# Performance work log

Hardware: AMD Instinct MI355X
Metric: run time of the kernel (lower is better)

## Reference

```python
import jax, jax.numpy as jnp
import numpy as np

N_NODES = 50000
N_EDGES = 800000
D_IN = 96
D_OUT = 96


def setup_inputs() -> dict:
    key = jax.random.key(0)
    k1, k2, k3, k4 = jax.random.split(key, 4)
    feat = jax.random.normal(k1, (N_NODES, D_IN), dtype=jnp.float32)
    # xavier_normal-like init for weight, zeros bias (as in the torch module)
    std = (2.0 / (D_IN + D_OUT)) ** 0.5
    weight = jax.random.normal(k2, (D_IN, D_OUT), dtype=jnp.float32) * std
    bias = jnp.zeros((D_OUT,), dtype=jnp.float32)
    src = jax.random.randint(k3, (N_EDGES,), 0, N_NODES, dtype=jnp.int64)
    dst = jax.random.randint(k4, (N_EDGES,), 0, N_NODES, dtype=jnp.int64)
    return {"feat": feat, "weight": weight, "bias": bias, "src": src, "dst": dst}


def reference(feat, weight, bias, src, dst):
    N = feat.shape[0]
    ones = jnp.ones(src.shape[0], dtype=feat.dtype)
    out_deg = jax.ops.segment_sum(ones, src, num_segments=N)  # out-degree per node
    in_deg = jax.ops.segment_sum(ones, dst, num_segments=N)   # in-degree per node
    ci = jnp.clip(out_deg, 1.0, None) ** -0.5                 # src-side norm
    cj = jnp.clip(in_deg, 1.0, None) ** -0.5                  # dst-side norm
    # gather src features * ci, scatter-sum to dst, scale by cj
    msg = feat[src] * ci[src, None]                           # [E, D_IN]
    agg = jax.ops.segment_sum(msg, dst, num_segments=N) * cj[:, None]
    # DGL UDF reduce only updates nodes that receive messages; isolated
    # (zero in-degree) nodes keep their original features.
    h = jnp.where(in_deg[:, None] > 0, agg, feat)
    return jnp.matmul(h, weight) + bias
```

## Files before the change

### kernel.cpp

```cpp
#include <hip/hip_runtime.h>

#define N_NODES 50000
#define N_EDGES 800000
#define D 96
#define D4 (D / 4)

#define HB 128
#define CHUNK (N_EDGES / HB)
#define NW (N_NODES / 4)

#define RL 12
#define NTILES (N_NODES / 16)
#define CONV_BLOCKS ((N_NODES * RL + 255) / 256)
#define WPREP_BLOCKS ((D * (D / 2) + 255) / 256)
#define CSR_CAP (N_EDGES + 8 * N_NODES)

typedef __attribute__((ext_vector_type(8))) short short8;
typedef __attribute__((ext_vector_type(4))) float floatx4;

__device__ __forceinline__ short8 as_short8(uint4 u) { return *(short8*)&u; }

__global__ void __launch_bounds__(1024) hist_kernel(
        const int* __restrict__ src, const int* __restrict__ dst,
        unsigned* __restrict__ hist, unsigned* __restrict__ total) {
    __shared__ unsigned hbin[NW];
    int b = blockIdx.x, t = threadIdx.x;
    if (b == 0 && t == 0) *total = 0;
    int e0 = b * CHUNK;
#pragma unroll 1
    for (int p = 0; p < 2; ++p) {
        const int* __restrict__ arr = (p == 0) ? src : dst;
        for (int i = t; i < NW; i += 1024) hbin[i] = 0;
        __syncthreads();
        for (int i = t; i < CHUNK; i += 1024) {
            int l = arr[e0 + i];
            atomicAdd(&hbin[l >> 2], 1u << ((l & 3) * 8));
        }
        __syncthreads();
        unsigned* __restrict__ g = hist + ((size_t)p * HB + b) * NW;
        for (int i = t; i < NW; i += 1024) g[i] = hbin[i];
        __syncthreads();
    }
}

__global__ void __launch_bounds__(256) reduce_kernel(
        unsigned* __restrict__ hist, float* __restrict__ ci,
        int* __restrict__ deg_in, int* __restrict__ off,
        unsigned* __restrict__ total) {
    int w = blockIdx.x * 256 + threadIdx.x;
    bool valid = w < NW;
    unsigned acc_s = 0;
    int4 dv = {0, 0, 0, 0};
    if (valid) {
        const unsigned* __restrict__ ps = hist + w;
        unsigned* __restrict__ pd = hist + (size_t)HB * NW + w;
#pragma unroll 8
        for (int b = 0; b < HB; ++b) acc_s += ps[(size_t)b * NW];
        unsigned run = 0;
#pragma unroll 4
        for (int b = 0; b < HB; ++b) {
            unsigned v = pd[(size_t)b * NW];
            pd[(size_t)b * NW] = run;
            run += v;
        }
        dv.x = (int)( run        & 0xFFu);
        dv.y = (int)((run >>  8) & 0xFFu);
        dv.z = (int)((run >> 16) & 0xFFu);
        dv.w = (int)( run >> 24        );
    }
    int4 pv;
    pv.x = (dv.x + 7) & ~7;
    pv.y = (dv.y + 7) & ~7;
    pv.z = (dv.z + 7) & ~7;
    pv.w = (dv.w + 7) & ~7;
    int sum4 = pv.x + pv.y + pv.z + pv.w;
    int lane = threadIdx.x & 63;
    int incl = sum4;
#pragma unroll
    for (int st = 1; st < 64; st <<= 1) {
        int v = __shfl_up(incl, st, 64);
        if (lane >= st) incl += v;
    }
    int excl = incl - sum4;
    int wave_total = __shfl(incl, 63, 64);
    int base = 0;
    if (lane == 63) base = (int)atomicAdd(total, (unsigned)wave_total);
    base = __shfl(base, 63, 64);
    if (valid) {
        int n0 = 4 * w;
        int b0 = base + excl;
        int4 ov;
        ov.x = b0;
        ov.y = b0 + pv.x;
        ov.z = b0 + pv.x + pv.y;
        ov.w = b0 + pv.x + pv.y + pv.z;
        *(int4*)&off[n0] = ov;
        *(int4*)&deg_in[n0] = dv;
        float4 cv;
        cv.x = rsqrtf(fmaxf((float)( acc_s        & 0xFFu), 1.0f));
        cv.y = rsqrtf(fmaxf((float)((acc_s >>  8) & 0xFFu), 1.0f));
        cv.z = rsqrtf(fmaxf((float)((acc_s >> 16) & 0xFFu), 1.0f));
        cv.w = rsqrtf(fmaxf((float)( acc_s >> 24        ), 1.0f));
        *(float4*)&ci[n0] = cv;
    }
}

__device__ __forceinline__ unsigned bf16pack(float a, float b) {
    unsigned ua = __float_as_uint(a);
    unsigned ub = __float_as_uint(b);
    ua = (ua + 0x7FFFu + ((ua >> 16) & 1u)) >> 16;
    ub = (ub + 0x7FFFu + ((ub >> 16) & 1u)) & 0xFFFF0000u;
    return ua | ub;
}

__global__ void __launch_bounds__(256) conv_kernel(
        const float4* __restrict__ feat4, const float* __restrict__ ci,
        uint4* __restrict__ sfeat, const float* __restrict__ W,
        unsigned* __restrict__ WT32) {
    int blk = blockIdx.x;
    if (blk >= CONV_BLOCKS) {
        int t = (blk - CONV_BLOCKS) * 256 + threadIdx.x;
        if (t >= D * (D / 2)) return;
        int n = t / (D / 2);
        int j = t - n * (D / 2);
        float w0 = W[(2 * j) * D + n];
        float w1 = W[(2 * j + 1) * D + n];
        WT32[n * (D / 2) + j] = bf16pack(w0, w1);
        return;
    }
    int t = blk * 256 + threadIdx.x;
    if (t >= N_NODES * RL) return;
    int n = t / RL;
    int lane = t - n * RL;
    float c = ci[n];
    float4 a = feat4[n * D4 + lane * 2];
    float4 b = feat4[n * D4 + lane * 2 + 1];
    uint4 o;
    o.x = bf16pack(a.x * c, a.y * c);
    o.y = bf16pack(a.z * c, a.w * c);
    o.z = bf16pack(b.x * c, b.y * c);
    o.w = bf16pack(b.z * c, b.w * c);
    sfeat[t] = o;
}

__global__ void __launch_bounds__(1024) fill_kernel(
        const int* __restrict__ src, const int* __restrict__ dst,
        const int* __restrict__ off, const unsigned* __restrict__ hist,
        unsigned short* __restrict__ csr) {
    __shared__ unsigned cur[NW];
    int b = blockIdx.x, t = threadIdx.x;
    const unsigned* __restrict__ pr = hist + ((size_t)HB + b) * NW;
    for (int i = t; i < NW; i += 1024) cur[i] = pr[i];
    __syncthreads();
    int e0 = b * CHUNK;
    for (int i = t; i < CHUNK; i += 1024) {
        int d = dst[e0 + i];
        int sh = (d & 3) * 8;
        unsigned old = atomicAdd(&cur[d >> 2], 1u << sh);
        int pos = (int)((old >> sh) & 0xFFu);
        csr[off[d] + pos] = (unsigned short)src[e0 + i];
    }
}

__global__ void __launch_bounds__(192) gather_kernel(
        const float4* __restrict__ feat4, const uint4* __restrict__ sfeat,
        const int* __restrict__ deg_in, const int* __restrict__ off,
        const unsigned short* __restrict__ csr, uint4* __restrict__ hbuf) {
    int tid = threadIdx.x;
    int g = tid / RL;
    int lane = tid - g * RL;
    int n = blockIdx.x * 16 + g;
    int deg = deg_in[n];
    uint4* __restrict__ hout = hbuf + (size_t)n * RL + lane;
    if (deg == 0) {
        float4 a = feat4[n * D4 + lane * 2];
        float4 b = feat4[n * D4 + lane * 2 + 1];
        uint4 o;
        o.x = bf16pack(a.x, a.y);
        o.y = bf16pack(a.z, a.w);
        o.z = bf16pack(b.x, b.y);
        o.w = bf16pack(b.z, b.w);
        *hout = o;
        return;
    }
    const unsigned short* __restrict__ bk = csr + off[n];
    const uint4* __restrict__ sf = sfeat + lane;
    float acc[8] = {};
#define ACC8(v)  { \
    acc[0] += __uint_as_float((v).x << 16); \
    acc[1] += __uint_as_float((v).x & 0xFFFF0000u); \
    acc[2] += __uint_as_float((v).y << 16); \
    acc[3] += __uint_as_float((v).y & 0xFFFF0000u); \
    acc[4] += __uint_as_float((v).z << 16); \
    acc[5] += __uint_as_float((v).z & 0xFFFF0000u); \
    acc[6] += __uint_as_float((v).w << 16); \
    acc[7] += __uint_as_float((v).w & 0xFFFF0000u); }
    int full = deg & ~7;
    int i = 0;
    for (; i < full; i += 8) {
        uint4 idx = *(const uint4*)(bk + i);
        unsigned s0 = idx.x & 0xFFFFu, s1 = idx.x >> 16;
        unsigned s2 = idx.y & 0xFFFFu, s3 = idx.y >> 16;
        unsigned s4 = idx.z & 0xFFFFu, s5 = idx.z >> 16;
        unsigned s6 = idx.w & 0xFFFFu, s7 = idx.w >> 16;
        uint4 v0 = sf[(size_t)s0 * RL];
        uint4 v1 = sf[(size_t)s1 * RL];
        uint4 v2 = sf[(size_t)s2 * RL];
        uint4 v3 = sf[(size_t)s3 * RL];
        uint4 v4 = sf[(size_t)s4 * RL];
        uint4 v5 = sf[(size_t)s5 * RL];
        uint4 v6 = sf[(size_t)s6 * RL];
        uint4 v7 = sf[(size_t)s7 * RL];
        ACC8(v0); ACC8(v1); ACC8(v2); ACC8(v3);
        ACC8(v4); ACC8(v5); ACC8(v6); ACC8(v7);
    }
    for (; i < deg; ++i) {
        uint4 v = sf[(size_t)bk[i] * RL];
        ACC8(v);
    }
#undef ACC8
    float cj = rsqrtf((float)deg);
    uint4 o;
    o.x = bf16pack(acc[0] * cj, acc[1] * cj);
    o.y = bf16pack(acc[2] * cj, acc[3] * cj);
    o.z = bf16pack(acc[4] * cj, acc[5] * cj);
    o.w = bf16pack(acc[6] * cj, acc[7] * cj);
    *hout = o;
}

__global__ void __launch_bounds__(256) mfma_mm_kernel(
        const uint4* __restrict__ hb4, const uint4* __restrict__ wt4,
        const float* __restrict__ bias, float* __restrict__ out) {
    int wave = threadIdx.x >> 6;
    int lane = threadIdx.x & 63;
    int tile = blockIdx.x * 4 + wave;
    if (tile >= NTILES) return;
    int m = lane & 15, quad = lane >> 4;
    int row0 = tile * 16;
    int rb = (row0 + m) * RL + quad;
    short8 a0 = as_short8(hb4[rb]);
    short8 a1 = as_short8(hb4[rb + 4]);
    short8 a2 = as_short8(hb4[rb + 8]);
    int r_out0 = row0 + quad * 4;
#pragma unroll
    for (int ct = 0; ct < 6; ++ct) {
        int n = ct * 16 + m;
        int wb = n * RL + quad;
        short8 b0 = as_short8(wt4[wb]);
        short8 b1 = as_short8(wt4[wb + 4]);
        short8 b2 = as_short8(wt4[wb + 8]);
        floatx4 c = {0.f, 0.f, 0.f, 0.f};
        c = __builtin_amdgcn_mfma_f32_16x16x32_bf16(a0, b0, c, 0, 0, 0);
        c = __builtin_amdgcn_mfma_f32_16x16x32_bf16(a1, b1, c, 0, 0, 0);
        c = __builtin_amdgcn_mfma_f32_16x16x32_bf16(a2, b2, c, 0, 0, 0);
        float bs = bias[n];
#pragma unroll
        for (int r = 0; r < 4; ++r)
            out[(size_t)(r_out0 + r) * D + n] = c[r] + bs;
    }
}

extern "C" void kernel_launch(void* const* d_in, const int* in_sizes, int n_in,
                              void* d_out, int out_size, void* d_ws, size_t ws_size,
                              hipStream_t stream) {
    const float* feat = (const float*)d_in[0];
    const float* W    = (const float*)d_in[1];
    const float* bias = (const float*)d_in[2];
    const int*   src  = (const int*)d_in[3];
    const int*   dst  = (const int*)d_in[4];

    unsigned*       hist   = (unsigned*)d_ws;
    float*          ci     = (float*)(hist + (size_t)2 * HB * NW);
    int*            off    = (int*)(ci + N_NODES);
    int*            deg_in = off + N_NODES;
    unsigned short* csr    = (unsigned short*)(deg_in + N_NODES);
    uint4*          sfeat  = (uint4*)((char*)csr + ((size_t)CSR_CAP * 2 + 15 & ~15));
    uint4*          hbuf   = sfeat + (size_t)N_NODES * RL;
    unsigned*       WT32   = (unsigned*)(hbuf + (size_t)N_NODES * RL);
    unsigned*       total  = WT32 + D * (D / 2);

    hist_kernel<<<HB, 1024, 0, stream>>>(src, dst, hist, total);
    reduce_kernel<<<(NW + 255) / 256, 256, 0, stream>>>(hist, ci, deg_in, off, total);
    conv_kernel<<<CONV_BLOCKS + WPREP_BLOCKS, 256, 0, stream>>>(
        (const float4*)feat, ci, sfeat, W, WT32);
    fill_kernel<<<HB, 1024, 0, stream>>>(src, dst, off, hist, csr);
    gather_kernel<<<N_NODES / 16, 192, 0, stream>>>(
        (const float4*)feat, sfeat, deg_in, off, csr, hbuf);
    mfma_mm_kernel<<<(NTILES + 3) / 4, 256, 0, stream>>>(
        hbuf, (const uint4*)WT32, bias, (float*)d_out);
}
```

Before: 159.7 us.

## Fuse reduce with feature conversion and gather with MFMA matmul

Merges the degree-reduce/offset kernel with the bf16 feature scaling pass, keeping ci in shared memory so the ci buffer round-trip and one launch go away. Also fuses the gather-aggregate with the MFMA matmul: each 192-thread block writes its 16 aggregated rows into padded LDS, and its 3 waves each compute 2 of the 6 output column tiles, so the hbuf buffer and another launch disappear. The trade-off is a reduce/convert kernel with only ~49 blocks, each converting 1024 nodes serially, which can cut parallelism for the streaming conversion. The gather blocks also now carry extra matmul work.

```diff
diff --git a/kernel.cpp b/kernel.cpp
--- a/kernel.cpp
+++ b/kernel.cpp
@@ -10,15 +10,22 @@
 #define NW (N_NODES / 4)
 
 #define RL 12
-#define NTILES (N_NODES / 16)
-#define CONV_BLOCKS ((N_NODES * RL + 255) / 256)
-#define WPREP_BLOCKS ((D * (D / 2) + 255) / 256)
+#define HPAD 13
+#define RC_BLOCKS ((NW + 255) / 256)
 #define CSR_CAP (N_EDGES + 8 * N_NODES)
 
 typedef __attribute__((ext_vector_type(8))) short short8;
 typedef __attribute__((ext_vector_type(4))) float floatx4;
 
 __device__ __forceinline__ short8 as_short8(uint4 u) { return *(short8*)&u; }
+
+__device__ __forceinline__ unsigned bf16pack(float a, float b) {
+    unsigned ua = __float_as_uint(a);
+    unsigned ub = __float_as_uint(b);
+    ua = (ua + 0x7FFFu + ((ua >> 16) & 1u)) >> 16;
+    ub = (ub + 0x7FFFu + ((ub >> 16) & 1u)) & 0xFFFF0000u;
+    return ua | ub;
+}
 
 __global__ void __launch_bounds__(1024) hist_kernel(
         const int* __restrict__ src, const int* __restrict__ dst,
@@ -43,11 +50,24 @@
     }
 }
 
-__global__ void __launch_bounds__(256) reduce_kernel(
-        unsigned* __restrict__ hist, float* __restrict__ ci,
-        int* __restrict__ deg_in, int* __restrict__ off,
-        unsigned* __restrict__ total) {
-    int w = blockIdx.x * 256 + threadIdx.x;
+__global__ void __launch_bounds__(256) reduce_conv_kernel(
+        unsigned* __restrict__ hist, const float4* __restrict__ feat4,
+        const float* __restrict__ W, int* __restrict__ deg_in,
+        int* __restrict__ off, unsigned* __restrict__ total,
+        uint4* __restrict__ sfeat, unsigned* __restrict__ WT32) {
+    int b = blockIdx.x, tid = threadIdx.x;
+    if (b == RC_BLOCKS) {
+        for (int t = tid; t < D * (D / 2); t += 256) {
+            int n = t / (D / 2);
+            int j = t - n * (D / 2);
+            float w0 = W[(2 * j) * D + n];
+            float w1 = W[(2 * j + 1) * D + n];
+            WT32[n * (D / 2) + j] = bf16pack(w0, w1);
+        }
+        return;
+    }
+    __shared__ float ci_s[1024];
+    int w = b * 256 + tid;
     bool valid = w < NW;
     unsigned acc_s = 0;
     int4 dv = {0, 0, 0, 0};
@@ -55,12 +75,12 @@
         const unsigned* __restrict__ ps = hist + w;
         unsigned* __restrict__ pd = hist + (size_t)HB * NW + w;
 #pragma unroll 8
-        for (int b = 0; b < HB; ++b) acc_s += ps[(size_t)b * NW];
+        for (int bb = 0; bb < HB; ++bb) acc_s += ps[(size_t)bb * NW];
         unsigned run = 0;
 #pragma unroll 4
-        for (int b = 0; b < HB; ++b) {
-            unsigned v = pd[(size_t)b * NW];
-            pd[(size_t)b * NW] = run;
+        for (int bb = 0; bb < HB; ++bb) {
+            unsigned v = pd[(size_t)bb * NW];
+            pd[(size_t)bb * NW] = run;
             run += v;
         }
         dv.x = (int)( run        & 0xFFu);
@@ -74,7 +94,7 @@
     pv.z = (dv.z + 7) & ~7;
     pv.w = (dv.w + 7) & ~7;
     int sum4 = pv.x + pv.y + pv.z + pv.w;
-    int lane = threadIdx.x & 63;
+    int lane = tid & 63;
     int incl = sum4;
 #pragma unroll
     for (int st = 1; st < 64; st <<= 1) {
@@ -101,46 +121,25 @@
         cv.y = rsqrtf(fmaxf((float)((acc_s >>  8) & 0xFFu), 1.0f));
         cv.z = rsqrtf(fmaxf((float)((acc_s >> 16) & 0xFFu), 1.0f));
         cv.w = rsqrtf(fmaxf((float)( acc_s >> 24        ), 1.0f));
-        *(float4*)&ci[n0] = cv;
-    }
-}
-
-__device__ __forceinline__ unsigned bf16pack(float a, float b) {
-    unsigned ua = __float_as_uint(a);
-    unsigned ub = __float_as_uint(b);
-    ua = (ua + 0x7FFFu + ((ua >> 16) & 1u)) >> 16;
-    ub = (ub + 0x7FFFu + ((ub >> 16) & 1u)) & 0xFFFF0000u;
-    return ua | ub;
-}
-
-__global__ void __launch_bounds__(256) conv_kernel(
-        const float4* __restrict__ feat4, const float* __restrict__ ci,
-        uint4* __restrict__ sfeat, const float* __restrict__ W,
-        unsigned* __restrict__ WT32) {
-    int blk = blockIdx.x;
-    if (blk >= CONV_BLOCKS) {
-        int t = (blk - CONV_BLOCKS) * 256 + threadIdx.x;
-        if (t >= D * (D / 2)) return;
-        int n = t / (D / 2);
-        int j = t - n * (D / 2);
-        float w0 = W[(2 * j) * D + n];
-        float w1 = W[(2 * j + 1) * D + n];
-        WT32[n * (D / 2) + j] = bf16pack(w0, w1);
-        return;
-    }
-    int t = blk * 256 + threadIdx.x;
-    if (t >= N_NODES * RL) return;
-    int n = t / RL;
-    int lane = t - n * RL;
-    float c = ci[n];
-    float4 a = feat4[n * D4 + lane * 2];
-    float4 b = feat4[n * D4 + lane * 2 + 1];
-    uint4 o;
-    o.x = bf16pack(a.x * c, a.y * c);
-    o.y = bf16pack(a.z * c, a.w * c);
-    o.z = bf16pack(b.x * c, b.y * c);
-    o.w = bf16pack(b.z * c, b.w * c);
-    sfeat[t] = o;
+        *(float4*)&ci_s[4 * tid] = cv;
+    }
+    __syncthreads();
+    int nbase = b * 1024;
+    int cnt = min(1024, N_NODES - nbase);
+    for (int i = tid; i < cnt * RL; i += 256) {
+        int nl = i / RL;
+        int lane2 = i - nl * RL;
+        int n = nbase + nl;
+        float c = ci_s[nl];
+        float4 a = feat4[n * D4 + lane2 * 2];
+        float4 bb = feat4[n * D4 + lane2 * 2 + 1];
+        uint4 o;
+        o.x = bf16pack(a.x * c, a.y * c);
+        o.y = bf16pack(a.z * c, a.w * c);
+        o.z = bf16pack(bb.x * c, bb.y * c);
+        o.w = bf16pack(bb.z * c, bb.w * c);
+        sfeat[(size_t)n * RL + lane2] = o;
+    }
 }
 
 __global__ void __launch_bounds__(1024) fill_kernel(
@@ -162,88 +161,85 @@
     }
 }
 
-__global__ void __launch_bounds__(192) gather_kernel(
+__global__ void __launch_bounds__(192) gather_mm_kernel(
         const float4* __restrict__ feat4, const uint4* __restrict__ sfeat,
         const int* __restrict__ deg_in, const int* __restrict__ off,
-        const unsigned short* __restrict__ csr, uint4* __restrict__ hbuf) {
+        const unsigned short* __restrict__ csr, const uint4* __restrict__ wt4,
+        const float* __restrict__ bias, float* __restrict__ out) {
+    __shared__ uint4 sh[16 * HPAD];
     int tid = threadIdx.x;
-    int g = tid / RL;
-    int lane = tid - g * RL;
-    int n = blockIdx.x * 16 + g;
-    int deg = deg_in[n];
-    uint4* __restrict__ hout = hbuf + (size_t)n * RL + lane;
-    if (deg == 0) {
-        float4 a = feat4[n * D4 + lane * 2];
-        float4 b = feat4[n * D4 + lane * 2 + 1];
-        uint4 o;
-        o.x = bf16pack(a.x, a.y);
-        o.y = bf16pack(a.z, a.w);
-        o.z = bf16pack(b.x, b.y);
-        o.w = bf16pack(b.z, b.w);
-        *hout = o;
-        return;
-    }
-    const unsigned short* __restrict__ bk = csr + off[n];
-    const uint4* __restrict__ sf = sfeat + lane;
-    float acc[8] = {};
+    {
+        int g = tid / RL;
+        int lane = tid - g * RL;
+        int n = blockIdx.x * 16 + g;
+        int deg = deg_in[n];
+        uint4* __restrict__ hout = &sh[g * HPAD + lane];
+        if (deg == 0) {
+            float4 a = feat4[n * D4 + lane * 2];
+            float4 b = feat4[n * D4 + lane * 2 + 1];
+            uint4 o;
+            o.x = bf16pack(a.x, a.y);
+            o.y = bf16pack(a.z, a.w);
+            o.z = bf16pack(b.x, b.y);
+            o.w = bf16pack(b.z, b.w);
+            *hout = o;
+        } else {
+            const unsigned short* __restrict__ bk = csr + off[n];
+            const uint4* __restrict__ sf = sfeat + lane;
+            float acc[8] = {};
 #define ACC8(v)  { \
-    acc[0] += __uint_as_float((v).x << 16); \
-    acc[1] += __uint_as_float((v).x & 0xFFFF0000u); \
-    acc[2] += __uint_as_float((v).y << 16); \
-    acc[3] += __uint_as_float((v).y & 0xFFFF0000u); \
-    acc[4] += __uint_as_float((v).z << 16); \
-    acc[5] += __uint_as_float((v).z & 0xFFFF0000u); \
-    acc[6] += __uint_as_float((v).w << 16); \
-    acc[7] += __uint_as_float((v).w & 0xFFFF0000u); }
-    int full = deg & ~7;
-    int i = 0;
-    for (; i < full; i += 8) {
-        uint4 idx = *(const uint4*)(bk + i);
-        unsigned s0 = idx.x & 0xFFFFu, s1 = idx.x >> 16;
-        unsigned s2 = idx.y & 0xFFFFu, s3 = idx.y >> 16;
-        unsigned s4 = idx.z & 0xFFFFu, s5 = idx.z >> 16;
-        unsigned s6 = idx.w & 0xFFFFu, s7 = idx.w >> 16;
-        uint4 v0 = sf[(size_t)s0 * RL];
-        uint4 v1 = sf[(size_t)s1 * RL];
-        uint4 v2 = sf[(size_t)s2 * RL];
-        uint4 v3 = sf[(size_t)s3 * RL];
-        uint4 v4 = sf[(size_t)s4 * RL];
-        uint4 v5 = sf[(size_t)s5 * RL];
-        uint4 v6 = sf[(size_t)s6 * RL];
-        uint4 v7 = sf[(size_t)s7 * RL];
-        ACC8(v0); ACC8(v1); ACC8(v2); ACC8(v3);
-        ACC8(v4); ACC8(v5); ACC8(v6); ACC8(v7);
-    }
-    for (; i < deg; ++i) {
-        uint4 v = sf[(size_t)bk[i] * RL];
-        ACC8(v);
-    }
+        acc[0] += __uint_as_float((v).x << 16); \
+        acc[1] += __uint_as_float((v).x & 0xFFFF0000u); \
+        acc[2] += __uint_as_float((v).y << 16); \
+        acc[3] += __uint_as_float((v).y & 0xFFFF0000u); \
+        acc[4] += __uint_as_float((v).z << 16); \
+        acc[5] += __uint_as_float((v).z & 0xFFFF0000u); \
+        acc[6] += __uint_as_float((v).w << 16); \
+        acc[7] += __uint_as_float((v).w & 0xFFFF0000u); }
+            int full = deg & ~7;
+            int i = 0;
+            for (; i < full; i += 8) {
+                uint4 idx = *(const uint4*)(bk + i);
+                unsigned s0 = idx.x & 0xFFFFu, s1 = idx.x >> 16;
+                unsigned s2 = idx.y & 0xFFFFu, s3 = idx.y >> 16;
+                unsigned s4 = idx.z & 0xFFFFu, s5 = idx.z >> 16;
+                unsigned s6 = idx.w & 0xFFFFu, s7 = idx.w >> 16;
+                uint4 v0 = sf[(size_t)s0 * RL];
+                uint4 v1 = sf[(size_t)s1 * RL];
+                uint4 v2 = sf[(size_t)s2 * RL];
+                uint4 v3 = sf[(size_t)s3 * RL];
+                uint4 v4 = sf[(size_t)s4 * RL];
+                uint4 v5 = sf[(size_t)s5 * RL];
+                uint4 v6 = sf[(size_t)s6 * RL];
+                uint4 v7 = sf[(size_t)s7 * RL];
+                ACC8(v0); ACC8(v1); ACC8(v2); ACC8(v3);
+                ACC8(v4); ACC8(v5); ACC8(v6); ACC8(v7);
+            }
+            for (; i < deg; ++i) {
+                uint4 v = sf[(size_t)bk[i] * RL];
+                ACC8(v);
+            }
 #undef ACC8
-    float cj = rsqrtf((float)deg);
-    uint4 o;
-    o.x = bf16pack(acc[0] * cj, acc[1] * cj);
-    o.y = bf16pack(acc[2] * cj, acc[3] * cj);
-    o.z = bf16pack(acc[4] * cj, acc[5] * cj);
-    o.w = bf16pack(acc[6] * cj, acc[7] * cj);
-    *hout = o;
-}
-
-__global__ void __launch_bounds__(256) mfma_mm_kernel(
-        const uint4* __restrict__ hb4, const uint4* __restrict__ wt4,
-        const float* __restrict__ bias, float* __restrict__ out) {
-    int wave = threadIdx.x >> 6;
-    int lane = threadIdx.x & 63;
-    int tile = blockIdx.x * 4 + wave;
-    if (tile >= NTILES) return;
+            float cj = rsqrtf((float)deg);
+            uint4 o;
+            o.x = bf16pack(acc[0] * cj, acc[1] * cj);
+            o.y = bf16pack(acc[2] * cj, acc[3] * cj);
+            o.z = bf16pack(acc[4] * cj, acc[5] * cj);
+            o.w = bf16pack(acc[6] * cj, acc[7] * cj);
+            *hout = o;
+        }
+    }
+    __syncthreads();
+    int wave = tid >> 6;
+    int lane = tid & 63;
     int m = lane & 15, quad = lane >> 4;
-    int row0 = tile * 16;
-    int rb = (row0 + m) * RL + quad;
-    short8 a0 = as_short8(hb4[rb]);
-    short8 a1 = as_short8(hb4[rb + 4]);
-    short8 a2 = as_short8(hb4[rb + 8]);
+    short8 a0 = as_short8(sh[m * HPAD + quad]);
+    short8 a1 = as_short8(sh[m * HPAD + 4 + quad]);
+    short8 a2 = as_short8(sh[m * HPAD + 8 + quad]);
+    int row0 = blockIdx.x * 16;
     int r_out0 = row0 + quad * 4;
 #pragma unroll
-    for (int ct = 0; ct < 6; ++ct) {
+    for (int ct = wave * 2; ct < wave * 2 + 2; ++ct) {
         int n = ct * 16 + m;
         int wb = n * RL + quad;
         short8 b0 = as_short8(wt4[wb]);
@@ -270,22 +266,18 @@
     const int*   dst  = (const int*)d_in[4];
 
     unsigned*       hist   = (unsigned*)d_ws;
-    float*          ci     = (float*)(hist + (size_t)2 * HB * NW);
-    int*            off    = (int*)(ci + N_NODES);
+    int*            off    = (int*)(hist + (size_t)2 * HB * NW);
     int*            deg_in = off + N_NODES;
     unsigned short* csr    = (unsigned short*)(deg_in + N_NODES);
-    uint4*          sfeat  = (uint4*)((char*)csr + ((size_t)CSR_CAP * 2 + 15 & ~15));
-    uint4*          hbuf   = sfeat + (size_t)N_NODES * RL;
-    unsigned*       WT32   = (unsigned*)(hbuf + (size_t)N_NODES * RL);
+    uint4*          sfeat  = (uint4*)((char*)csr + (((size_t)CSR_CAP * 2 + 15) & ~(size_t)15));
+    unsigned*       WT32   = (unsigned*)(sfeat + (size_t)N_NODES * RL);
     unsigned*       total  = WT32 + D * (D / 2);
 
     hist_kernel<<<HB, 1024, 0, stream>>>(src, dst, hist, total);
-    reduce_kernel<<<(NW + 255) / 256, 256, 0, stream>>>(hist, ci, deg_in, off, total);
-    conv_kernel<<<CONV_BLOCKS + WPREP_BLOCKS, 256, 0, stream>>>(
-        (const float4*)feat, ci, sfeat, W, WT32);
+    reduce_conv_kernel<<<RC_BLOCKS + 1, 256, 0, stream>>>(
+        hist, (const float4*)feat, W, deg_in, off, total, sfeat, WT32);
     fill_kernel<<<HB, 1024, 0, stream>>>(src, dst, off, hist, csr);
-    gather_kernel<<<N_NODES / 16, 192, 0, stream>>>(
-        (const float4*)feat, sfeat, deg_in, off, csr, hbuf);
-    mfma_mm_kernel<<<(NTILES + 3) / 4, 256, 0, stream>>>(
-        hbuf, (const uint4*)WT32, bias, (float*)d_out);
-}
+    gather_mm_kernel<<<N_NODES / 16, 192, 0, stream>>>(
+        (const float4*)feat, sfeat, deg_in, off, csr, (const uint4*)WT32,
+        bias, (float*)d_out);
+}
```

New measurement: 167.8 us. 5.1% more time.

## Fuse neighbor gather with MFMA projection through shared memory tile

Applied to the files above, without the earlier changes.

The gather kernel now writes its 16-node bf16 aggregate tile into padded shared memory instead of a global buffer. After a barrier, its three waves each compute two 16-column MFMA output tiles, which removes the separate matmul kernel launch and the global round trip of the hidden features. The reduce kernel also moves from 256 to 64 threads per block, so each block is a single wave. The cost is that the matmul work now sits behind the gather's tail latency inside each block, with three waves instead of four per tile.

```diff
diff --git a/kernel.cpp b/kernel.cpp
--- a/kernel.cpp
+++ b/kernel.cpp
@@ -10,7 +10,7 @@
 #define NW (N_NODES / 4)
 
 #define RL 12
-#define NTILES (N_NODES / 16)
+#define HPAD 13
 #define CONV_BLOCKS ((N_NODES * RL + 255) / 256)
 #define WPREP_BLOCKS ((D * (D / 2) + 255) / 256)
 #define CSR_CAP (N_EDGES + 8 * N_NODES)
@@ -19,6 +19,14 @@
 typedef __attribute__((ext_vector_type(4))) float floatx4;
 
 __device__ __forceinline__ short8 as_short8(uint4 u) { return *(short8*)&u; }
+
+__device__ __forceinline__ unsigned bf16pack(float a, float b) {
+    unsigned ua = __float_as_uint(a);
+    unsigned ub = __float_as_uint(b);
+    ua = (ua + 0x7FFFu + ((ua >> 16) & 1u)) >> 16;
+    ub = (ub + 0x7FFFu + ((ub >> 16) & 1u)) & 0xFFFF0000u;
+    return ua | ub;
+}
 
 __global__ void __launch_bounds__(1024) hist_kernel(
         const int* __restrict__ src, const int* __restrict__ dst,
@@ -43,11 +51,11 @@
     }
 }
 
-__global__ void __launch_bounds__(256) reduce_kernel(
+__global__ void __launch_bounds__(64) reduce_kernel(
         unsigned* __restrict__ hist, float* __restrict__ ci,
         int* __restrict__ deg_in, int* __restrict__ off,
         unsigned* __restrict__ total) {
-    int w = blockIdx.x * 256 + threadIdx.x;
+    int w = blockIdx.x * 64 + threadIdx.x;
     bool valid = w < NW;
     unsigned acc_s = 0;
     int4 dv = {0, 0, 0, 0};
@@ -74,7 +82,7 @@
     pv.z = (dv.z + 7) & ~7;
     pv.w = (dv.w + 7) & ~7;
     int sum4 = pv.x + pv.y + pv.z + pv.w;
-    int lane = threadIdx.x & 63;
+    int lane = threadIdx.x;
     int incl = sum4;
 #pragma unroll
     for (int st = 1; st < 64; st <<= 1) {
@@ -105,14 +113,6 @@
     }
 }
 
-__device__ __forceinline__ unsigned bf16pack(float a, float b) {
-    unsigned ua = __float_as_uint(a);
-    unsigned ub = __float_as_uint(b);
-    ua = (ua + 0x7FFFu + ((ua >> 16) & 1u)) >> 16;
-    ub = (ub + 0x7FFFu + ((ub >> 16) & 1u)) & 0xFFFF0000u;
-    return ua | ub;
-}
-
 __global__ void __launch_bounds__(256) conv_kernel(
         const float4* __restrict__ feat4, const float* __restrict__ ci,
         uint4* __restrict__ sfeat, const float* __restrict__ W,
@@ -162,88 +162,85 @@
     }
 }
 
-__global__ void __launch_bounds__(192) gather_kernel(
+__global__ void __launch_bounds__(192) gather_mm_kernel(
         const float4* __restrict__ feat4, const uint4* __restrict__ sfeat,
         const int* __restrict__ deg_in, const int* __restrict__ off,
-        const unsigned short* __restrict__ csr, uint4* __restrict__ hbuf) {
+        const unsigned short* __restrict__ csr, const uint4* __restrict__ wt4,
+        const float* __restrict__ bias, float* __restrict__ out) {
+    __shared__ uint4 sh[16 * HPAD];
     int tid = threadIdx.x;
-    int g = tid / RL;
-    int lane = tid - g * RL;
-    int n = blockIdx.x * 16 + g;
-    int deg = deg_in[n];
-    uint4* __restrict__ hout = hbuf + (size_t)n * RL + lane;
-    if (deg == 0) {
-        float4 a = feat4[n * D4 + lane * 2];
-        float4 b = feat4[n * D4 + lane * 2 + 1];
-        uint4 o;
-        o.x = bf16pack(a.x, a.y);
-        o.y = bf16pack(a.z, a.w);
-        o.z = bf16pack(b.x, b.y);
-        o.w = bf16pack(b.z, b.w);
-        *hout = o;
-        return;
-    }
-    const unsigned short* __restrict__ bk = csr + off[n];
-    const uint4* __restrict__ sf = sfeat + lane;
-    float acc[8] = {};
+    {
+        int g = tid / RL;
+        int lane = tid - g * RL;
+        int n = blockIdx.x * 16 + g;
+        int deg = deg_in[n];
+        uint4* __restrict__ hout = &sh[g * HPAD + lane];
+        if (deg == 0) {
+            float4 a = feat4[n * D4 + lane * 2];
+            float4 b = feat4[n * D4 + lane * 2 + 1];
+            uint4 o;
+            o.x = bf16pack(a.x, a.y);
+            o.y = bf16pack(a.z, a.w);
+            o.z = bf16pack(b.x, b.y);
+            o.w = bf16pack(b.z, b.w);
+            *hout = o;
+        } else {
+            const unsigned short* __restrict__ bk = csr + off[n];
+            const uint4* __restrict__ sf = sfeat + lane;
+            float acc[8] = {};
 #define ACC8(v)  { \
-    acc[0] += __uint_as_float((v).x << 16); \
-    acc[1] += __uint_as_float((v).x & 0xFFFF0000u); \
-    acc[2] += __uint_as_float((v).y << 16); \
-    acc[3] += __uint_as_float((v).y & 0xFFFF0000u); \
-    acc[4] += __uint_as_float((v).z << 16); \
-    acc[5] += __uint_as_float((v).z & 0xFFFF0000u); \
-    acc[6] += __uint_as_float((v).w << 16); \
-    acc[7] += __uint_as_float((v).w & 0xFFFF0000u); }
-    int full = deg & ~7;
-    int i = 0;
-    for (; i < full; i += 8) {
-        uint4 idx = *(const uint4*)(bk + i);
-        unsigned s0 = idx.x & 0xFFFFu, s1 = idx.x >> 16;
-        unsigned s2 = idx.y & 0xFFFFu, s3 = idx.y >> 16;
-        unsigned s4 = idx.z & 0xFFFFu, s5 = idx.z >> 16;
-        unsigned s6 = idx.w & 0xFFFFu, s7 = idx.w >> 16;
-        uint4 v0 = sf[(size_t)s0 * RL];
-        uint4 v1 = sf[(size_t)s1 * RL];
-        uint4 v2 = sf[(size_t)s2 * RL];
-        uint4 v3 = sf[(size_t)s3 * RL];
-        uint4 v4 = sf[(size_t)s4 * RL];
-        uint4 v5 = sf[(size_t)s5 * RL];
-        uint4 v6 = sf[(size_t)s6 * RL];
-        uint4 v7 = sf[(size_t)s7 * RL];
-        ACC8(v0); ACC8(v1); ACC8(v2); ACC8(v3);
-        ACC8(v4); ACC8(v5); ACC8(v6); ACC8(v7);
-    }
-    for (; i < deg; ++i) {
-        uint4 v = sf[(size_t)bk[i] * RL];
-        ACC8(v);
-    }
+        acc[0] += __uint_as_float((v).x << 16); \
+        acc[1] += __uint_as_float((v).x & 0xFFFF0000u); \
+        acc[2] += __uint_as_float((v).y << 16); \
+        acc[3] += __uint_as_float((v).y & 0xFFFF0000u); \
+        acc[4] += __uint_as_float((v).z << 16); \
+        acc[5] += __uint_as_float((v).z & 0xFFFF0000u); \
+        acc[6] += __uint_as_float((v).w << 16); \
+        acc[7] += __uint_as_float((v).w & 0xFFFF0000u); }
+            int full = deg & ~7;
+            int i = 0;
+            for (; i < full; i += 8) {
+                uint4 idx = *(const uint4*)(bk + i);
+                unsigned s0 = idx.x & 0xFFFFu, s1 = idx.x >> 16;
+                unsigned s2 = idx.y & 0xFFFFu, s3 = idx.y >> 16;
+                unsigned s4 = idx.z & 0xFFFFu, s5 = idx.z >> 16;
+                unsigned s6 = idx.w & 0xFFFFu, s7 = idx.w >> 16;
+                uint4 v0 = sf[(size_t)s0 * RL];
+                uint4 v1 = sf[(size_t)s1 * RL];
+                uint4 v2 = sf[(size_t)s2 * RL];
+                uint4 v3 = sf[(size_t)s3 * RL];
+                uint4 v4 = sf[(size_t)s4 * RL];
+                uint4 v5 = sf[(size_t)s5 * RL];
+                uint4 v6 = sf[(size_t)s6 * RL];
+                uint4 v7 = sf[(size_t)s7 * RL];
+                ACC8(v0); ACC8(v1); ACC8(v2); ACC8(v3);
+                ACC8(v4); ACC8(v5); ACC8(v6); ACC8(v7);
+            }
+            for (; i < deg; ++i) {
+                uint4 v = sf[(size_t)bk[i] * RL];
+                ACC8(v);
+            }
 #undef ACC8
-    float cj = rsqrtf((float)deg);
-    uint4 o;
-    o.x = bf16pack(acc[0] * cj, acc[1] * cj);
-    o.y = bf16pack(acc[2] * cj, acc[3] * cj);
-    o.z = bf16pack(acc[4] * cj, acc[5] * cj);
-    o.w = bf16pack(acc[6] * cj, acc[7] * cj);
-    *hout = o;
-}
-
-__global__ void __launch_bounds__(256) mfma_mm_kernel(
-        const uint4* __restrict__ hb4, const uint4* __restrict__ wt4,
-        const float* __restrict__ bias, float* __restrict__ out) {
-    int wave = threadIdx.x >> 6;
-    int lane = threadIdx.x & 63;
-    int tile = blockIdx.x * 4 + wave;
-    if (tile >= NTILES) return;
+            float cj = rsqrtf((float)deg);
+            uint4 o;
+            o.x = bf16pack(acc[0] * cj, acc[1] * cj);
+            o.y = bf16pack(acc[2] * cj, acc[3] * cj);
+            o.z = bf16pack(acc[4] * cj, acc[5] * cj);
+            o.w = bf16pack(acc[6] * cj, acc[7] * cj);
+            *hout = o;
+        }
+    }
+    __syncthreads();
+    int wave = tid >> 6;
+    int lane = tid & 63;
     int m = lane & 15, quad = lane >> 4;
-    int row0 = tile * 16;
-    int rb = (row0 + m) * RL + quad;
-    short8 a0 = as_short8(hb4[rb]);
-    short8 a1 = as_short8(hb4[rb + 4]);
-    short8 a2 = as_short8(hb4[rb + 8]);
+    short8 a0 = as_short8(sh[m * HPAD + quad]);
+    short8 a1 = as_short8(sh[m * HPAD + 4 + quad]);
+    short8 a2 = as_short8(sh[m * HPAD + 8 + quad]);
+    int row0 = blockIdx.x * 16;
     int r_out0 = row0 + quad * 4;
 #pragma unroll
-    for (int ct = 0; ct < 6; ++ct) {
+    for (int ct = wave * 2; ct < wave * 2 + 2; ++ct) {
         int n = ct * 16 + m;
         int wb = n * RL + quad;
         short8 b0 = as_short8(wt4[wb]);
@@ -274,18 +271,16 @@
     int*            off    = (int*)(ci + N_NODES);
     int*            deg_in = off + N_NODES;
     unsigned short* csr    = (unsigned short*)(deg_in + N_NODES);
-    uint4*          sfeat  = (uint4*)((char*)csr + ((size_t)CSR_CAP * 2 + 15 & ~15));
-    uint4*          hbuf   = sfeat + (size_t)N_NODES * RL;
-    unsigned*       WT32   = (unsigned*)(hbuf + (size_t)N_NODES * RL);
+    uint4*          sfeat  = (uint4*)((char*)csr + (((size_t)CSR_CAP * 2 + 15) & ~(size_t)15));
+    unsigned*       WT32   = (unsigned*)(sfeat + (size_t)N_NODES * RL);
     unsigned*       total  = WT32 + D * (D / 2);
 
     hist_kernel<<<HB, 1024, 0, stream>>>(src, dst, hist, total);
-    reduce_kernel<<<(NW + 255) / 256, 256, 0, stream>>>(hist, ci, deg_in, off, total);
+    reduce_kernel<<<(NW + 63) / 64, 64, 0, stream>>>(hist, ci, deg_in, off, total);
     conv_kernel<<<CONV_BLOCKS + WPREP_BLOCKS, 256, 0, stream>>>(
         (const float4*)feat, ci, sfeat, W, WT32);
     fill_kernel<<<HB, 1024, 0, stream>>>(src, dst, off, hist, csr);
-    gather_kernel<<<N_NODES / 16, 192, 0, stream>>>(
-        (const float4*)feat, sfeat, deg_in, off, csr, hbuf);
-    mfma_mm_kernel<<<(NTILES + 3) / 4, 256, 0, stream>>>(
-        hbuf, (const uint4*)WT32, bias, (float*)d_out);
-}
+    gather_mm_kernel<<<N_NODES / 16, 192, 0, stream>>>(
+        (const float4*)feat, sfeat, deg_in, off, csr, (const uint4*)WT32,
+        bias, (float*)d_out);
+}
```

New measurement: 155.3 us. -2.8%, faster.
